# Performance work log

Measured on AMD Instinct MI355X. Metric: run time of the kernel, lower is better.

The kernel has to match this reference:

```python
import jax, jax.numpy as jnp
import numpy as np
import math

B, T, E = 1, 2048, 1024
H = 8                      # num_heads
D = E // H // 2            # head_dim = 64
LAMBDA_INIT = 0.8 - 0.6 * math.exp(-0.3 * 1)  # depth=1
SCALE_BASE = 512.0
THETA = 10000.0


def _rope_tables(T, d):
    # lucidrains rotary-embedding-torch, use_xpos=True, interleaved pairs
    inv_freq = 1.0 / (THETA ** (jnp.arange(0, d, 2, dtype=jnp.float32) / d))
    pos = jnp.arange(T, dtype=jnp.float32)
    freqs = pos[:, None] * inv_freq[None, :]            # (T, d/2)
    freqs = jnp.repeat(freqs, 2, axis=-1)               # (T, d) interleaved
    sv = (jnp.arange(0, d, 2, dtype=jnp.float32) + 0.4 * d) / (1.4 * d)
    power = (pos - T // 2) / SCALE_BASE
    scale = sv[None, :] ** power[:, None]               # (T, d/2)
    scale = jnp.concatenate([scale, scale], axis=-1)    # (T, d)
    return freqs, scale


def _rotate_half(x):
    # interleaved rotate: (..., d) pairs (x1, x2) -> (-x2, x1)
    x1 = x[..., 0::2]
    x2 = x[..., 1::2]
    return jnp.stack([-x2, x1], axis=-1).reshape(x.shape)


def _apply_rope(t, freqs, scale):
    # t: (B, T, h, d); freqs/scale: (T, d) broadcast over heads
    f = freqs[None, :, None, :]
    s = scale[None, :, None, :]
    return t * jnp.cos(f) * s + _rotate_half(t) * jnp.sin(f) * s


def setup_inputs() -> dict:
    key = jax.random.key(0)
    ks = jax.random.split(key, 9)
    w = 0.02
    return {
        "x": jax.random.normal(ks[0], (B, T, E), dtype=jnp.float32),
        "Wq": jax.random.normal(ks[1], (E, E), dtype=jnp.float32) * w,
        "Wk": jax.random.normal(ks[2], (E, E), dtype=jnp.float32) * w,
        "Wv": jax.random.normal(ks[3], (E, E), dtype=jnp.float32) * w,
        "Wo": jax.random.normal(ks[4], (E, E), dtype=jnp.float32) * w,
        "lambda_q1": jax.random.normal(ks[5], (D,), dtype=jnp.float32) * 0.1,
        "lambda_k1": jax.random.normal(ks[6], (D,), dtype=jnp.float32) * 0.1,
        "lambda_q2": jax.random.normal(ks[7], (D,), dtype=jnp.float32) * 0.1,
        "lambda_k2": jax.random.normal(ks[8], (D,), dtype=jnp.float32) * 0.1,
    }


def reference(x, Wq, Wk, Wv, Wo, lambda_q1, lambda_k1, lambda_q2, lambda_k2):
    b, t, e = x.shape
    scaling = D ** -0.5

    q = (x @ Wq.T).reshape(b, t, 2 * H, D)
    k = (x @ Wk.T).reshape(b, t, 2 * H, D)   # n_rep = 1
    v = (x @ Wv.T).reshape(b, t, H, 2 * D)

    freqs, scale = _rope_tables(t, D)
    q = _apply_rope(q, freqs, scale)
    k = _apply_rope(k, freqs, 1.0 / scale)   # xpos: keys use scale**-1

    q = jnp.transpose(q, (0, 2, 1, 3)) * scaling   # (B, 2H, T, D)
    k = jnp.transpose(k, (0, 2, 1, 3))             # (B, 2H, T, D)
    v = jnp.transpose(v, (0, 2, 1, 3))             # (B, H, T, 2D)

    scores = jnp.einsum('bhtd,bhsd->bhts', q, k)
    probs = jax.nn.softmax(scores.astype(jnp.float32), axis=-1).astype(scores.dtype)

    lam1 = jnp.exp(jnp.sum(lambda_q1 * lambda_k1))
    lam2 = jnp.exp(jnp.sum(lambda_q2 * lambda_k2))
    lam = lam1 - lam2 + LAMBDA_INIT

    probs = probs.reshape(b, H, 2, t, t)
    diff = probs[:, :, 0] - lam * probs[:, :, 1]   # (B, H, T, T)

    attn = jnp.einsum('bhts,bhsd->bhtd', diff, v)  # (B, H, T, 2D)
    # RMSNorm (no affine), eps=1e-5
    attn = attn * jax.lax.rsqrt(jnp.mean(attn * attn, axis=-1, keepdims=True) + 1e-5)
    attn = attn * (1.0 - LAMBDA_INIT)

    attn = jnp.transpose(attn, (0, 2, 1, 3)).reshape(b, t, e)
    return attn @ Wo.T
```

## Files before the change

### kernel.cpp

```cpp
#include <hip/hip_runtime.h>
#include <hip/hip_bf16.h>

typedef __hip_bfloat16 bf16;
typedef _Float16 f16;
typedef __attribute__((ext_vector_type(8))) __bf16 bf16x8;
typedef __attribute__((ext_vector_type(8))) _Float16 f16x8;
typedef __attribute__((ext_vector_type(4))) _Float16 f16x4;
typedef __attribute__((ext_vector_type(4))) float floatx4;
typedef __attribute__((ext_vector_type(16))) float floatx16;

#define T_SEQ 2048
#define EMB   1024
#define LAMBDA_INIT 0.35550906759096926f

__device__ __forceinline__ bf16 f2bf(float f) {
  unsigned u;
  __builtin_memcpy(&u, &f, 4);
  u += 0x7FFF + ((u >> 16) & 1);
  unsigned short h = (unsigned short)(u >> 16);
  bf16 r;
  __builtin_memcpy(&r, &h, 2);
  return r;
}

__device__ __forceinline__ int cvtpk_bf16(float lo, float hi) {
  int r;
  asm("v_cvt_pk_bf16_f32 %0, %1, %2" : "=v"(r) : "v"(lo), "v"(hi));
  return r;
}

__device__ __forceinline__ void permswap(int& a, int& b) {
  asm volatile("v_permlane32_swap_b32 %0, %1" : "+v"(a), "+v"(b));
}

__device__ __forceinline__ void gl_lds16(const void* g, void* l) {
  __builtin_amdgcn_global_load_lds((const __attribute__((address_space(1))) void*)g,
                                   (__attribute__((address_space(3))) void*)l, 16, 0, 0);
}

__device__ __forceinline__ floatx4 mfma_h(f16x8 a, f16x8 b, floatx4 c) {
  return __builtin_amdgcn_mfma_f32_16x16x32_f16(a, b, c, 0, 0, 0);
}
__device__ __forceinline__ floatx16 mfma32_h(f16x8 a, f16x8 b, floatx16 c) {
  return __builtin_amdgcn_mfma_f32_32x32x16_f16(a, b, c, 0, 0, 0);
}
__device__ __forceinline__ floatx16 mfma32_bf(bf16x8 a, bf16x8 b, floatx16 c) {
  return __builtin_amdgcn_mfma_f32_32x32x16_bf16(a, b, c, 0, 0, 0);
}

__global__ __launch_bounds__(256) void convert_kernel(
    const float* __restrict__ x,  const float* __restrict__ wq,
    const float* __restrict__ wk, const float* __restrict__ wv,
    const float* __restrict__ wo,
    f16* __restrict__ xf, f16* __restrict__ wqf, f16* __restrict__ wkf,
    f16* __restrict__ wvf, f16* __restrict__ wof)
{
  int b = blockIdx.x;
  const float* src; f16* dst; long off;
  if      (b < 2048) { src = x;  dst = xf;  off = (long)b * 1024; }
  else if (b < 3072) { src = wq; dst = wqf; off = (long)(b - 2048) * 1024; }
  else if (b < 4096) { src = wk; dst = wkf; off = (long)(b - 3072) * 1024; }
  else if (b < 5120) { src = wv; dst = wvf; off = (long)(b - 4096) * 1024; }
  else               { src = wo; dst = wof; off = (long)(b - 5120) * 1024; }
  long i = off + threadIdx.x * 4;
  float4 v = *(const float4*)(src + i);
  f16x4 o;
  o.x = (f16)v.x; o.y = (f16)v.y; o.z = (f16)v.z; o.w = (f16)v.w;
  *(f16x4*)(dst + i) = o;
}

template <int MODE>
__device__ __forceinline__ void gemm64x128_f16(
    const f16* __restrict__ A_, const f16* __restrict__ B_,
    void* C0v, int Kld, int Klen, int ldc, int m0, int n0, char* smem)
{
  f16* As = (f16*)smem;
  f16* Bs = (f16*)(smem + 8192);
  const int tid  = threadIdx.x;
  const int wave = tid >> 6, lane = tid & 63, quad = lane >> 4, l16 = lane & 15;
  const int mo = (wave & 1) << 5;
  const int no = (wave >> 1) << 6;

  floatx4 acc[2][4];
  #pragma unroll
  for (int i = 0; i < 2; i++)
    #pragma unroll
    for (int j = 0; j < 4; j++) { acc[i][j][0]=0.f; acc[i][j][1]=0.f; acc[i][j][2]=0.f; acc[i][j][3]=0.f; }

  const int srow = tid >> 3;
  const int ch   = (tid & 7) ^ (srow & 7);
  const long aoff = (long)(m0 + srow) * Kld + ch * 8;
  const long boff = (long)(n0 + srow) * Kld + ch * 8;
  const int wb = wave << 10;

  for (int k0 = 0; k0 < Klen; k0 += 64) {
    #pragma unroll
    for (int rr = 0; rr < 2; rr++)
      gl_lds16(A_ + aoff + k0 + (long)rr * 32 * Kld, smem + wb + rr * 4096);
    #pragma unroll
    for (int rr = 0; rr < 4; rr++)
      gl_lds16(B_ + boff + k0 + (long)rr * 32 * Kld, smem + 8192 + wb + rr * 4096);
    __syncthreads();
    #pragma unroll
    for (int kt = 0; kt < 2; kt++) {
      f16x8 a[2], b[4];
      #pragma unroll
      for (int i = 0; i < 2; i++) {
        int m = mo + i * 16 + l16;
        a[i] = *(const f16x8*)(As + m * 64 + ((((kt << 2) | quad) ^ (m & 7)) << 3));
      }
      #pragma unroll
      for (int j = 0; j < 4; j++) {
        int n = no + j * 16 + l16;
        b[j] = *(const f16x8*)(Bs + n * 64 + ((((kt << 2) | quad) ^ (n & 7)) << 3));
      }
      #pragma unroll
      for (int i = 0; i < 2; i++)
        #pragma unroll
        for (int j = 0; j < 4; j++)
          acc[i][j] = mfma_h(a[i], b[j], acc[i][j]);
    }
    __syncthreads();
  }

  if (MODE == 1) {
    #pragma unroll
    for (int i = 0; i < 2; i++)
      #pragma unroll
      for (int j = 0; j < 4; j++)
        #pragma unroll
        for (int r = 0; r < 4; r++) {
          int row = m0 + mo + i * 16 + quad * 4 + r;
          int col = n0 + no + j * 16 + l16;
          ((float*)C0v)[(long)row * ldc + col] = acc[i][j][r];
        }
  } else {
    unsigned short* E = (unsigned short*)smem;
    #pragma unroll
    for (int i = 0; i < 2; i++)
      #pragma unroll
      for (int j = 0; j < 4; j++)
        #pragma unroll
        for (int r = 0; r < 4; r++) {
          int row = mo + i * 16 + quad * 4 + r;
          int col = no + j * 16 + l16;
          float v = acc[i][j][r];
          unsigned short bits;
          if (MODE == 0) {
            bf16 t = f2bf(v);
            __builtin_memcpy(&bits, &t, 2);
          } else {
            float p = __shfl_xor(v, 1, 64);
            int d = col & 63;
            float fr = (float)(m0 + row) * __expf((float)(d >> 1) * -0.28782313662425574f);
            float sn, cs;
            sincosf(fr, &sn, &cs);
            float rot = (col & 1) ? fmaf(v, cs, p * sn) : fmaf(v, cs, -p * sn);
            float power = (float)(m0 + row - 1024) * (1.0f / 512.0f);
            if (MODE == 3) power = -power;
            float sv = fmaf(2.0f, (float)(d & 31), 25.6f) * (1.0f / 89.6f);
            float s = __expf(power * __logf(sv));
            float ov = rot * s;
            if (MODE == 2) ov *= 0.125f;
            f16 t = (f16)ov;
            __builtin_memcpy(&bits, &t, 2);
          }
          E[row * 128 + col] = bits;
        }
    __syncthreads();
    const int rr0 = tid >> 4;
    const int c8  = (tid & 15) * 8;
    #pragma unroll
    for (int p2 = 0; p2 < 4; p2++) {
      int row = p2 * 16 + rr0;
      *(uint4*)((unsigned short*)C0v + (long)(m0 + row) * ldc + n0 + c8) =
          *(const uint4*)(E + row * 128 + c8);
    }
  }
}

__global__ __launch_bounds__(256) void qkv_gemm(
    const f16* __restrict__ xf,
    const f16* __restrict__ wqf, const f16* __restrict__ wkf,
    const f16* __restrict__ wvf,
    f16* __restrict__ qf, f16* __restrict__ kf, bf16* __restrict__ vt)
{
  __shared__ char smem[24576];
  int bid = blockIdx.x;
  if (bid < 256) {
    gemm64x128_f16<2>(xf, wqf, qf, 1024, 1024, 1024, (bid >> 3) * 64, (bid & 7) * 128, smem);
  } else if (bid < 512) {
    bid -= 256;
    gemm64x128_f16<3>(xf, wkf, kf, 1024, 1024, 1024, (bid >> 3) * 64, (bid & 7) * 128, smem);
  } else {
    bid -= 512;
    gemm64x128_f16<0>(wvf, xf, vt, 1024, 1024, 2048, (bid >> 4) * 64, (bid & 15) * 128, smem);
  }
}

__global__ __launch_bounds__(256) void out_gemm(const f16* __restrict__ attn,
                                                const f16* __restrict__ Wo,
                                                float* __restrict__ p0,
                                                float* __restrict__ p1)
{
  __shared__ char smem[24576];
  int bid = blockIdx.x;
  const int kh = bid >> 8;
  const int b  = bid & 255;
  float* pb = kh ? p1 : p0;
  gemm64x128_f16<1>(attn + kh * 512, Wo + kh * 512, pb, 1024, 512, 1024,
                    (b >> 3) * 64, (b & 7) * 128, smem);
}

__global__ __launch_bounds__(256) void add_out(const float* __restrict__ p0,
                                               const float* __restrict__ p1,
                                               float* __restrict__ out)
{
  long i = ((long)blockIdx.x * 256 + threadIdx.x) * 4;
  float4 a = *(const float4*)(p0 + i);
  float4 b = *(const float4*)(p1 + i);
  float4 c;
  c.x = a.x + b.x; c.y = a.y + b.y; c.z = a.z + b.z; c.w = a.w + b.w;
  *(float4*)(out + i) = c;
}

__global__ __launch_bounds__(256) void diff_attn(
    const f16* __restrict__ qf_, const f16* __restrict__ kf_,
    const bf16* __restrict__ vt,
    const float* __restrict__ lq1, const float* __restrict__ lk1,
    const float* __restrict__ lq2, const float* __restrict__ lk2,
    f16* __restrict__ attn)
{
  __shared__ char smem[65536];
  const int tid  = threadIdx.x;
  const int wave = tid >> 6, lane = tid & 63;
  const int l32 = lane & 31, lh = lane >> 5;
  const int h  = blockIdx.x & 7;
  const int qb = blockIdx.x >> 3;
  const int hl = wave >> 1;
  const int ws = wave & 1;
  const int hh = h * 2 + hl;
  const int t0 = qb * 32;

  float a1 = lq1[lane] * lk1[lane];
  float a2 = lq2[lane] * lk2[lane];
  #pragma unroll
  for (int off = 1; off < 64; off <<= 1) {
    a1 += __shfl_xor(a1, off, 64);
    a2 += __shfl_xor(a2, off, 64);
  }
  const float lam = __expf(a1) - __expf(a2) + LAMBDA_INIT;

  f16x8 qfr[4];
  {
    const f16* qrow = qf_ + (long)(t0 + l32) * EMB + hh * 64 + lh * 8;
    #pragma unroll
    for (int kt = 0; kt < 4; kt++) qfr[kt] = *(const f16x8*)(qrow + kt * 16);
  }

  floatx16 o[4];
  #pragma unroll
  for (int nt = 0; nt < 4; nt++)
    #pragma unroll
    for (int r = 0; r < 16; r++) o[nt][r] = 0.f;
  float lr0 = 0.f, lr1 = 0.f, lr2 = 0.f, lr3 = 0.f;

  const int srow = lane >> 3;
  const int ch   = (lane & 7) ^ srow;
  const f16*  kgp = kf_ + (long)(h * 2 + ws) * 64 + (long)srow * EMB + ch * 8;
  const bf16* vgp = vt + (long)(h * 128 + (wave - 2) * 64 + srow) * T_SEQ + ch * 8;
  const int kofs = wave * 8192;
  const int vofs = 16384 + (wave - 2) * 8192;

  if (wave < 2) {
    #pragma unroll
    for (int j = 0; j < 8; j++)
      gl_lds16(kgp + (long)j * 8 * EMB, smem + kofs + j * 1024);
  } else {
    #pragma unroll
    for (int j = 0; j < 8; j++)
      gl_lds16(vgp + (long)j * 8 * T_SEQ, smem + vofs + j * 1024);
  }

  for (int kb = 0; kb < T_SEQ; kb += 64) {
    const int cur = (kb >> 6) & 1;
    const char* sb = smem + cur * 32768;

    asm volatile("s_waitcnt vmcnt(0)" ::: "memory");
    asm volatile("s_barrier" ::: "memory");

    const f16*  Ks  = (const f16*)(sb + hl * 8192);
    const bf16* Vsb = (const bf16*)(sb + 16384);

    f16x8 kfr[4];
    #pragma unroll
    for (int kt = 0; kt < 4; kt++) {
      int krow = ws * 32 + l32;
      int c = kt * 2 + lh;
      kfr[kt] = *(const f16x8*)(Ks + krow * 64 + ((c ^ (krow & 7)) << 3));
    }
    bf16x8 vfr[4][2];
    #pragma unroll
    for (int nt = 0; nt < 4; nt++) {
      #pragma unroll
      for (int kt = 0; kt < 2; kt++) {
        int vrow = nt * 32 + l32;
        int c = ws * 4 + kt * 2 + lh;
        vfr[nt][kt] = *(const bf16x8*)(Vsb + vrow * 64 + ((c ^ (vrow & 7)) << 3));
      }
    }

    if (kb + 64 < T_SEQ) {
      char* nb = smem + (cur ^ 1) * 32768;
      if (wave < 2) {
        #pragma unroll
        for (int j = 0; j < 8; j++)
          gl_lds16(kgp + (long)(kb + 64) * EMB + (long)j * 8 * EMB,
                   nb + kofs + j * 1024);
      } else {
        #pragma unroll
        for (int j = 0; j < 8; j++)
          gl_lds16(vgp + (kb + 64) + (long)j * 8 * T_SEQ,
                   nb + vofs + j * 1024);
      }
    }

    floatx16 s;
    #pragma unroll
    for (int r = 0; r < 16; r++) s[r] = 0.f;
    #pragma unroll
    for (int kt = 0; kt < 4; kt++)
      s = mfma32_h(kfr[kt], qfr[kt], s);
    #pragma unroll
    for (int r = 0; r < 4; r++) {
      float p0 = __builtin_amdgcn_exp2f(
          fmaf(s[r], 1.4426950408889634f, -17.312340490667562f));
      float p1 = __builtin_amdgcn_exp2f(
          fmaf(s[r + 4], 1.4426950408889634f, -17.312340490667562f));
      float p2 = __builtin_amdgcn_exp2f(
          fmaf(s[r + 8], 1.4426950408889634f, -17.312340490667562f));
      float p3 = __builtin_amdgcn_exp2f(
          fmaf(s[r + 12], 1.4426950408889634f, -17.312340490667562f));
      s[r] = p0; s[r + 4] = p1; s[r + 8] = p2; s[r + 12] = p3;
      lr0 += p0; lr1 += p1; lr2 += p2; lr3 += p3;
    }
    bf16x8 pf[2];
    #pragma unroll
    for (int kt = 0; kt < 2; kt++) {
      const int b0 = kt * 8;
      int w0 = cvtpk_bf16(s[b0 + 0], s[b0 + 1]);
      int w1 = cvtpk_bf16(s[b0 + 2], s[b0 + 3]);
      int w2 = cvtpk_bf16(s[b0 + 4], s[b0 + 5]);
      int w3 = cvtpk_bf16(s[b0 + 6], s[b0 + 7]);
      permswap(w0, w2);
      permswap(w1, w3);
      union { int i[4]; bf16x8 v; } u;
      u.i[0] = w0; u.i[1] = w1; u.i[2] = w2; u.i[3] = w3;
      pf[kt] = u.v;
    }
    #pragma unroll
    for (int nt = 0; nt < 4; nt++) {
      #pragma unroll
      for (int kt = 0; kt < 2; kt++)
        o[nt] = mfma32_bf(pf[kt], vfr[nt][kt], o[nt]);
    }
  }
  __syncthreads();

  float lr = (lr0 + lr1) + (lr2 + lr3);
  float lrw = lr + __shfl_xor(lr, 32, 64);

  float* Cb = (float*)smem;
  float* Lb = (float*)(smem + 32768);

  if (ws == 1) {
    #pragma unroll
    for (int r = 0; r < 16; r++) {
      int m = (r & 3) + 8 * (r >> 2) + 4 * lh;
      #pragma unroll
      for (int nt = 0; nt < 4; nt++)
        Cb[hl * 4096 + m * 128 + nt * 32 + l32] = o[nt][r];
    }
  }
  if (lh == 0) Lb[ws * 64 + hl * 32 + l32] = lrw;
  __syncthreads();
  if (ws == 0) {
    #pragma unroll
    for (int r = 0; r < 16; r++) {
      int m = (r & 3) + 8 * (r >> 2) + 4 * lh;
      float inv = 1.0f / (Lb[hl * 32 + m] + Lb[64 + hl * 32 + m]);
      #pragma unroll
      for (int nt = 0; nt < 4; nt++)
        o[nt][r] = (o[nt][r] + Cb[hl * 4096 + m * 128 + nt * 32 + l32]) * inv;
    }
  }
  __syncthreads();
  if (hl == 1 && ws == 0) {
    #pragma unroll
    for (int r = 0; r < 16; r++) {
      int m = (r & 3) + 8 * (r >> 2) + 4 * lh;
      #pragma unroll
      for (int nt = 0; nt < 4; nt++)
        Cb[4096 + m * 128 + nt * 32 + l32] = o[nt][r];
    }
  }
  __syncthreads();
  if (hl == 0 && ws == 0) {
    float ss[16];
    #pragma unroll
    for (int r = 0; r < 16; r++) {
      int m = (r & 3) + 8 * (r >> 2) + 4 * lh;
      ss[r] = 0.f;
      #pragma unroll
      for (int nt = 0; nt < 4; nt++) {
        float v = o[nt][r] - lam * Cb[4096 + m * 128 + nt * 32 + l32];
        o[nt][r] = v;
        ss[r] += v * v;
      }
    }
    #pragma unroll
    for (int r = 0; r < 16; r++) {
      ss[r] += __shfl_xor(ss[r], 1, 64);
      ss[r] += __shfl_xor(ss[r], 2, 64);
      ss[r] += __shfl_xor(ss[r], 4, 64);
      ss[r] += __shfl_xor(ss[r], 8, 64);
      ss[r] += __shfl_xor(ss[r], 16, 64);
      float rms = rsqrtf(ss[r] * (1.0f / 128.0f) + 1e-5f) * (1.0f - LAMBDA_INIT);
      int m = (r & 3) + 8 * (r >> 2) + 4 * lh;
      #pragma unroll
      for (int nt = 0; nt < 4; nt++)
        attn[(long)(t0 + m) * EMB + h * 128 + nt * 32 + l32] = (f16)(o[nt][r] * rms);
    }
  }
}

extern "C" void kernel_launch(void* const* d_in, const int* in_sizes, int n_in,
                              void* d_out, int out_size, void* d_ws, size_t ws_size,
                              hipStream_t stream)
{
  (void)in_sizes; (void)n_in; (void)out_size; (void)ws_size;
  const float* x   = (const float*)d_in[0];
  const float* Wq  = (const float*)d_in[1];
  const float* Wk  = (const float*)d_in[2];
  const float* Wv  = (const float*)d_in[3];
  const float* Wo  = (const float*)d_in[4];
  const float* lq1 = (const float*)d_in[5];
  const float* lk1 = (const float*)d_in[6];
  const float* lq2 = (const float*)d_in[7];
  const float* lk2 = (const float*)d_in[8];
  float* out = (float*)d_out;

  const size_t TM = (size_t)T_SEQ * EMB;
  const size_t WM = (size_t)EMB * EMB;
  bf16* vtws = (bf16*)d_ws;
  f16*  aws  = (f16*)(vtws + TM);
  f16*  xf   = aws  + TM;
  f16*  wqf  = xf   + TM;
  f16*  wkf  = wqf  + WM;
  f16*  wvf  = wkf  + WM;
  f16*  wof  = wvf  + WM;
  f16*  qf   = wof  + WM;
  f16*  kf   = qf   + TM;

  float* p0 = (float*)xf;
  float* p1 = (float*)qf;

  convert_kernel<<<6144, 256, 0, stream>>>(x, Wq, Wk, Wv, Wo,
                                           xf, wqf, wkf, wvf, wof);
  qkv_gemm<<<768, 256, 0, stream>>>(xf, wqf, wkf, wvf, qf, kf, vtws);
  diff_attn<<<512, 256, 0, stream>>>(qf, kf, vtws, lq1, lk1, lq2, lk2, aws);
  out_gemm<<<512, 256, 0, stream>>>(aws, wof, p0, p1);
  add_out<<<2048, 256, 0, stream>>>(p0, p1, out);
}
```

Before: 170.7 us.

## Double-buffer LDS tiles in the f16 GEMM to overlap loads with MFMA

The shared 64x128 GEMM helper now uses two LDS stages. The next K-tile's global-to-LDS copy is issued after the current tile's fragments are loaded into registers and before the MFMAs run, which replaces the two __syncthreads per iteration with one waitcnt plus barrier. The aim is to hide global load latency behind the MFMA work in the QKV and output projections. In exchange, LDS per block doubles to 48 KB, which can lower the number of resident blocks per CU.

```diff
diff --git a/kernel.cpp b/kernel.cpp
--- a/kernel.cpp
+++ b/kernel.cpp
@@ -74,8 +74,6 @@
     const f16* __restrict__ A_, const f16* __restrict__ B_,
     void* C0v, int Kld, int Klen, int ldc, int m0, int n0, char* smem)
 {
-  f16* As = (f16*)smem;
-  f16* Bs = (f16*)(smem + 8192);
   const int tid  = threadIdx.x;
   const int wave = tid >> 6, lane = tid & 63, quad = lane >> 4, l16 = lane & 15;
   const int mo = (wave & 1) << 5;
@@ -93,35 +91,57 @@
   const long boff = (long)(n0 + srow) * Kld + ch * 8;
   const int wb = wave << 10;
 
+  #pragma unroll
+  for (int rr = 0; rr < 2; rr++)
+    gl_lds16(A_ + aoff + (long)rr * 32 * Kld, smem + wb + rr * 4096);
+  #pragma unroll
+  for (int rr = 0; rr < 4; rr++)
+    gl_lds16(B_ + boff + (long)rr * 32 * Kld, smem + 8192 + wb + rr * 4096);
+
   for (int k0 = 0; k0 < Klen; k0 += 64) {
-    #pragma unroll
-    for (int rr = 0; rr < 2; rr++)
-      gl_lds16(A_ + aoff + k0 + (long)rr * 32 * Kld, smem + wb + rr * 4096);
-    #pragma unroll
-    for (int rr = 0; rr < 4; rr++)
-      gl_lds16(B_ + boff + k0 + (long)rr * 32 * Kld, smem + 8192 + wb + rr * 4096);
-    __syncthreads();
+    const int cur = (k0 >> 6) & 1;
+    const char* sb = smem + cur * 24576;
+
+    asm volatile("s_waitcnt vmcnt(0)" ::: "memory");
+    asm volatile("s_barrier" ::: "memory");
+
+    const f16* As = (const f16*)sb;
+    const f16* Bs = (const f16*)(sb + 8192);
+
+    f16x8 a[2][2], b[2][4];
     #pragma unroll
     for (int kt = 0; kt < 2; kt++) {
-      f16x8 a[2], b[4];
       #pragma unroll
       for (int i = 0; i < 2; i++) {
         int m = mo + i * 16 + l16;
-        a[i] = *(const f16x8*)(As + m * 64 + ((((kt << 2) | quad) ^ (m & 7)) << 3));
+        a[kt][i] = *(const f16x8*)(As + m * 64 + ((((kt << 2) | quad) ^ (m & 7)) << 3));
       }
       #pragma unroll
       for (int j = 0; j < 4; j++) {
         int n = no + j * 16 + l16;
-        b[j] = *(const f16x8*)(Bs + n * 64 + ((((kt << 2) | quad) ^ (n & 7)) << 3));
+        b[kt][j] = *(const f16x8*)(Bs + n * 64 + ((((kt << 2) | quad) ^ (n & 7)) << 3));
       }
+    }
+
+    if (k0 + 64 < Klen) {
+      char* nb = smem + (cur ^ 1) * 24576;
+      #pragma unroll
+      for (int rr = 0; rr < 2; rr++)
+        gl_lds16(A_ + aoff + k0 + 64 + (long)rr * 32 * Kld, nb + wb + rr * 4096);
+      #pragma unroll
+      for (int rr = 0; rr < 4; rr++)
+        gl_lds16(B_ + boff + k0 + 64 + (long)rr * 32 * Kld, nb + 8192 + wb + rr * 4096);
+    }
+
+    #pragma unroll
+    for (int kt = 0; kt < 2; kt++)
       #pragma unroll
       for (int i = 0; i < 2; i++)
         #pragma unroll
         for (int j = 0; j < 4; j++)
-          acc[i][j] = mfma_h(a[i], b[j], acc[i][j]);
-    }
-    __syncthreads();
-  }
+          acc[i][j] = mfma_h(a[kt][i], b[kt][j], acc[i][j]);
+  }
+  __syncthreads();
 
   if (MODE == 1) {
     #pragma unroll
@@ -185,7 +205,7 @@
     const f16* __restrict__ wvf,
     f16* __restrict__ qf, f16* __restrict__ kf, bf16* __restrict__ vt)
 {
-  __shared__ char smem[24576];
+  __shared__ char smem[49152];
   int bid = blockIdx.x;
   if (bid < 256) {
     gemm64x128_f16<2>(xf, wqf, qf, 1024, 1024, 1024, (bid >> 3) * 64, (bid & 7) * 128, smem);
@@ -203,7 +223,7 @@
                                                 float* __restrict__ p0,
                                                 float* __restrict__ p1)
 {
-  __shared__ char smem[24576];
+  __shared__ char smem[49152];
   int bid = blockIdx.x;
   const int kh = bid >> 8;
   const int b  = bid & 255;
```

After: 191.1 us. +11.9%, slower.
